# Kernel tuning notes

Hardware: AMD Instinct MI355X
Metric: run time of the kernel (lower is better)

Reference implementation:

```python
import jax, jax.numpy as jnp
import numpy as np
from jax import lax

B, C, K = 16, 320, 8  # batch, channels, template kernel size
EPS = 1e-12  # F.normalize eps


def _pool_to(x, k):
    # adaptive avg pool to (k, k); H, W are exact multiples of k here
    b, c, h, w = x.shape
    return x.reshape(b, c, k, h // k, k, w // k).mean(axis=(3, 5))


def _l2norm(x):
    # L2 normalize over channel dim (dim=1), matching F.normalize(p=2, dim=1)
    n = jnp.sqrt(jnp.sum(x * x, axis=1, keepdims=True))
    return x / jnp.maximum(n, EPS)


def _fusion(feats, w1, b1, w2, b2):
    # global avg pool -> 2-layer MLP score per template -> softmax -> weighted sum
    scores = jnp.concatenate(
        [jax.nn.relu(f.mean(axis=(2, 3)) @ w1 + b1) @ w2 + b2 for f in feats], axis=1
    )  # (B, 3)
    a = jax.nn.softmax(scores, axis=1)
    return sum(a[:, i, None, None, None] * feats[i] for i in range(3))


def _corr(template_kernel, search):
    # depthwise correlation + channel sum == per-sample VALID conv with a
    # single (1, C, K, K) kernel; vmap over batch
    tn = _l2norm(template_kernel)  # (B, C, K, K)
    sn = _l2norm(search)           # (B, C, H, W)

    def one(sb, tb):
        return lax.conv_general_dilated(
            sb[None], tb[None], (1, 1), 'VALID',
            dimension_numbers=('NCHW', 'OIHW', 'NCHW'))[0]  # (1, Ho, Wo)

    return jax.vmap(one)(sn, tn)  # (B, 1, Ho, Wo)


_SPECS = [
    ('t0_p3', (B, C, 32, 32)), ('t0_p4', (B, C, 16, 16)), ('t0_p5', (B, C, 8, 8)),
    ('t1_p3', (B, C, 32, 32)), ('t1_p4', (B, C, 16, 16)), ('t1_p5', (B, C, 8, 8)),
    ('t2_p3', (B, C, 32, 32)), ('t2_p4', (B, C, 16, 16)), ('t2_p5', (B, C, 8, 8)),
    ('s_p3', (B, C, 64, 64)), ('s_p4', (B, C, 32, 32)), ('s_p5', (B, C, 16, 16)),
]
_PARAMS = [
    ('fp3_w1', (C, C // 4)), ('fp3_b1', (C // 4,)), ('fp3_w2', (C // 4, 1)), ('fp3_b2', (1,)),
    ('fp4_w1', (C, C // 4)), ('fp4_b1', (C // 4,)), ('fp4_w2', (C // 4, 1)), ('fp4_b2', (1,)),
    ('fp5_w1', (C, C // 4)), ('fp5_b1', (C // 4,)), ('fp5_w2', (C // 4, 1)), ('fp5_b2', (1,)),
]


def setup_inputs() -> dict:
    key = jax.random.key(0)
    d = {}
    for i, (name, shape) in enumerate(_SPECS):
        d[name] = jax.random.normal(jax.random.fold_in(key, i), shape, jnp.float32)
    for j, (name, shape) in enumerate(_PARAMS):
        k = jax.random.fold_in(key, 100 + j)
        if name.endswith('b1') or name.endswith('b2'):
            d[name] = jnp.zeros(shape, jnp.float32)
        else:
            d[name] = jax.random.normal(k, shape, jnp.float32) * 0.05
    return d


def reference(t0_p3, t0_p4, t0_p5, t1_p3, t1_p4, t1_p5, t2_p3, t2_p4, t2_p5,
              s_p3, s_p4, s_p5,
              fp3_w1, fp3_b1, fp3_w2, fp3_b2,
              fp4_w1, fp4_b1, fp4_w2, fp4_b2,
              fp5_w1, fp5_b1, fp5_w2, fp5_b2):
    tp3 = _fusion([t0_p3, t1_p3, t2_p3], fp3_w1, fp3_b1, fp3_w2, fp3_b2)
    tp4 = _fusion([t0_p4, t1_p4, t2_p4], fp4_w1, fp4_b1, fp4_w2, fp4_b2)
    tp5 = _fusion([t0_p5, t1_p5, t2_p5], fp5_w1, fp5_b1, fp5_w2, fp5_b2)
    corr_p3 = _corr(_pool_to(tp3, K), s_p3)  # (B, 1, 57, 57)
    corr_p4 = _corr(_pool_to(tp4, K), s_p4)  # (B, 1, 25, 25)
    corr_p5 = _corr(_pool_to(tp5, K), s_p5)  # (B, 1, 9, 9)
    return (corr_p3, corr_p4, corr_p5)
```

## Files before the change

### kernel.cpp

```cpp
#include <hip/hip_runtime.h>
#include <math.h>

#define BATCH 16
#define CH 320

typedef __attribute__((ext_vector_type(8))) short bf16x8;
typedef __attribute__((ext_vector_type(4))) float f32x4;

union AFrag { bf16x8 f; unsigned q[4]; };

static constexpr size_t PLSZ     = (size_t)BATCH * CH * 64;
static constexpr size_t WS_POOL3 = 0;
static constexpr size_t WS_POOL4 = 3 * PLSZ;
static constexpr size_t WS_TF    = 6 * PLSZ;
static constexpr size_t WS_MEANS = 9 * PLSZ;
static constexpr size_t WS_AW    = WS_MEANS + 9 * BATCH * CH;
static constexpr size_t WS_PART  = WS_AW + 144;
static constexpr size_t WS_ABF   = WS_PART + 3 * BATCH * 80 * 64;
static constexpr size_t UB3 = 0;
static constexpr size_t UB4 = (size_t)BATCH * 4096 * 64;
static constexpr size_t UB5 = UB4 + (size_t)BATCH * 1024 * 64;

__device__ __forceinline__ float bf2f(unsigned short u) {
    union { unsigned int i; float f; } x; x.i = ((unsigned int)u) << 16; return x.f;
}
__device__ __forceinline__ unsigned short f2bf(float f) {
    union { float f; unsigned int i; } x; x.f = f;
    return (unsigned short)((x.i + 0x7FFFu + ((x.i >> 16) & 1u)) >> 16);
}
__device__ __forceinline__ unsigned cvtpk(float lo, float hi) {
    unsigned r;
    asm("v_cvt_pk_bf16_f32 %0, %1, %2" : "=v"(r) : "v"(lo), "v"(hi));
    return r;
}

template <int HW, int KK>
__device__ __forceinline__ void pool_body(int idx, const float* __restrict__ a0,
                                          const float* __restrict__ a1, const float* __restrict__ a2,
                                          float* __restrict__ dst, float* __restrict__ means, int lane) {
    constexpr int NPL = BATCH * CH * 64;
    int tmpl = idx / NPL;
    int r = idx % NPL;
    const float* src = (tmpl == 0) ? a0 : ((tmpl == 1) ? a1 : a2);
    int bc = r >> 6;
    int pos = r & 63;
    int oh = pos >> 3, ow = pos & 7;
    const float* base = src + (size_t)bc * HW * HW;
    float s = 0.0f;
    if constexpr (KK == 4) {
#pragma unroll
        for (int i = 0; i < 4; ++i) {
            float4 v = *(const float4*)(base + (oh * 4 + i) * HW + ow * 4);
            s += v.x + v.y + v.z + v.w;
        }
    } else {
#pragma unroll
        for (int i = 0; i < 2; ++i) {
            float2 v = *(const float2*)(base + (oh * 2 + i) * HW + ow * 2);
            s += v.x + v.y;
        }
    }
    s *= (1.0f / (KK * KK));
    dst[idx] = s;
    float m = s;
#pragma unroll
    for (int o = 32; o; o >>= 1) m += __shfl_xor(m, o);
    if (lane == 0) means[tmpl * (BATCH * CH) + bc] = m * (1.0f / 64.0f);
}

__global__ __launch_bounds__(256) void prep_kernel(
    const float* __restrict__ t0p3, const float* __restrict__ t1p3, const float* __restrict__ t2p3,
    const float* __restrict__ t0p4, const float* __restrict__ t1p4, const float* __restrict__ t2p4,
    const float* __restrict__ t0p5, const float* __restrict__ t1p5, const float* __restrict__ t2p5,
    float* __restrict__ pool3, float* __restrict__ pool4, float* __restrict__ means) {
    int bid = blockIdx.x, t = threadIdx.x, lane = t & 63;
    if (bid < 3840) {
        pool_body<32, 4>(bid * 256 + t, t0p3, t1p3, t2p3, pool3, means, lane);
    } else if (bid < 7680) {
        pool_body<16, 2>((bid - 3840) * 256 + t, t0p4, t1p4, t2p4, pool4, means + 3 * BATCH * CH, lane);
    } else {
        int w = ((bid - 7680) * 256 + t) >> 6;
        constexpr int NR = BATCH * CH;
        int tmpl = w / NR, rem = w % NR;
        const float* src = (tmpl == 0) ? t0p5 : ((tmpl == 1) ? t1p5 : t2p5);
        float v = src[(size_t)rem * 64 + lane];
#pragma unroll
        for (int o = 32; o; o >>= 1) v += __shfl_xor(v, o);
        if (lane == 0) means[6 * BATCH * CH + w] = v * (1.0f / 64.0f);
    }
}

__global__ __launch_bounds__(256) void weights_kernel(const float* __restrict__ means,
        const float* w13, const float* b13, const float* w23, const float* b23,
        const float* w14, const float* b14, const float* w24, const float* b24,
        const float* w15, const float* b15, const float* w25, const float* b25,
        float* __restrict__ a_out) {
    __shared__ float m[3 * CH];
    __shared__ float hv[240];
    __shared__ float sc[3];
    int lvl = blockIdx.x / BATCH;
    int b = blockIdx.x % BATCH;
    int t = threadIdx.x;
    const float* w1 = (lvl == 0) ? w13 : ((lvl == 1) ? w14 : w15);
    const float* b1 = (lvl == 0) ? b13 : ((lvl == 1) ? b14 : b15);
    const float* w2 = (lvl == 0) ? w23 : ((lvl == 1) ? w24 : w25);
    const float* b2 = (lvl == 0) ? b23 : ((lvl == 1) ? b24 : b25);
    const float* mb = means + lvl * (3 * BATCH * CH);
    for (int j = t; j < 3 * CH; j += 256) {
        int i = j / CH, c = j % CH;
        m[j] = mb[i * (BATCH * CH) + b * CH + c];
    }
    __syncthreads();
    if (t < 240) {
        int i = t / 80, jj = t % 80;
        float acc = b1[jj];
#pragma unroll 4
        for (int c = 0; c < CH; ++c) acc = fmaf(m[i * CH + c], w1[c * 80 + jj], acc);
        hv[t] = fmaxf(acc, 0.0f) * w2[jj];
    }
    __syncthreads();
    if (t < 3) {
        float s = b2[0];
#pragma unroll 8
        for (int jj = 0; jj < 80; ++jj) s += hv[t * 80 + jj];
        sc[t] = s;
    }
    __syncthreads();
    if (t == 0) {
        float mx = fmaxf(sc[0], fmaxf(sc[1], sc[2]));
        float e0 = expf(sc[0] - mx), e1 = expf(sc[1] - mx), e2 = expf(sc[2] - mx);
        float inv = 1.0f / (e0 + e1 + e2);
        float* ao = a_out + lvl * 48 + b * 3;
        ao[0] = e0 * inv; ao[1] = e1 * inv; ao[2] = e2 * inv;
    }
}

__global__ __launch_bounds__(256) void fuse_kernel(
        const float* __restrict__ p30, const float* __restrict__ p31, const float* __restrict__ p32,
        const float* __restrict__ p40, const float* __restrict__ p41, const float* __restrict__ p42,
        const float* __restrict__ p50, const float* __restrict__ p51, const float* __restrict__ p52,
        const float* __restrict__ aw, float* __restrict__ tf, float* __restrict__ partial) {
    __shared__ float red[256];
    int lvl = blockIdx.x / 1280;
    int r = blockIdx.x % 1280;
    int t = threadIdx.x;
    const float* p0 = (lvl == 0) ? p30 : ((lvl == 1) ? p40 : p50);
    const float* p1 = (lvl == 0) ? p31 : ((lvl == 1) ? p41 : p51);
    const float* p2 = (lvl == 0) ? p32 : ((lvl == 1) ? p42 : p52);
    int idx = r * 256 + t;
    int b = r / 80;
    int j = r % 80;
    const float* ab = aw + lvl * 48 + b * 3;
    float a0 = ab[0], a1 = ab[1], a2 = ab[2];
    float v = a0 * p0[idx] + a1 * p1[idx] + a2 * p2[idx];
    tf[(size_t)lvl * PLSZ + idx] = v;
    red[t] = v * v;
    __syncthreads();
    if (t < 64) {
        float s = red[t] + red[t + 64] + red[t + 128] + red[t + 192];
        partial[((size_t)(lvl * BATCH + b) * 80 + j) * 64 + t] = s;
    }
}

__global__ __launch_bounds__(256) void atrans_kernel(const float* __restrict__ tf,
        const float* __restrict__ part, short* __restrict__ abf) {
    __shared__ float lds[64 * 68];
    __shared__ float red2[4 * 64];
    __shared__ float sv[64];
    int lvl = blockIdx.x >> 4;
    int b = blockIdx.x & 15;
    int t = threadIdx.x;
    {
        const float* p = part + ((size_t)(lvl * BATCH + b) * 80) * 64 + (t & 63);
        int jg = t >> 6;
        float s = 0.0f;
        for (int j = jg * 20; j < jg * 20 + 20; ++j) s += p[j * 64];
        red2[jg * 64 + (t & 63)] = s;
    }
    __syncthreads();
    if (t < 64) {
        float s = red2[t] + red2[64 + t] + red2[128 + t] + red2[192 + t];
        sv[t] = 1.0f / fmaxf(sqrtf(s), 1e-12f);
    }
    __syncthreads();
    const float* tb = tf + (size_t)lvl * PLSZ + (size_t)b * (CH * 64);
    short* ab = abf + ((size_t)(lvl * BATCH + b) * 64) * 320;
    for (int c0 = 0; c0 < 320; c0 += 64) {
        __syncthreads();
#pragma unroll
        for (int i = 0; i < 4; ++i) {
            int c = (t >> 4) + 16 * i;
            int p4 = (t & 15) * 4;
            *(float4*)(lds + c * 68 + p4) = *(const float4*)(tb + (size_t)(c0 + c) * 64 + p4);
        }
        __syncthreads();
        int p = t >> 2;
        int cs = (t & 3) * 16;
        float s_p = sv[p];
        bf16x8 o0, o1;
#pragma unroll
        for (int u = 0; u < 8; ++u) o0[u] = (short)f2bf(lds[(cs + u) * 68 + p] * s_p);
#pragma unroll
        for (int u = 0; u < 8; ++u) o1[u] = (short)f2bf(lds[(cs + 8 + u) * 68 + p] * s_p);
        *(bf16x8*)(ab + (size_t)p * 320 + c0 + cs) = o0;
        *(bf16x8*)(ab + (size_t)p * 320 + c0 + cs + 8) = o1;
    }
}

template <int H>
__device__ __forceinline__ void gemm_body(const float* __restrict__ S, const short* __restrict__ T,
                                          short* __restrict__ V, int bid) {
    constexpr int N = H * H;
    constexpr int XB = N / 64;
    int b = bid / XB;
    int x0b = (bid % XB) * 64;
    int t = threadIdx.x;
    int w = t >> 6, l = t & 63, g = l >> 4, ln = l & 15;
    int xw = x0b + 16 * w;

    const float* Sb = S + (size_t)b * CH * N + xw + ln;
    const short* Tb = T + (size_t)b * 64 * 320;

    f32x4 acc[4];
#pragma unroll
    for (int i = 0; i < 4; ++i) acc[i] = (f32x4){0.f, 0.f, 0.f, 0.f};
    float ssq = 0.0f;

#pragma unroll
    for (int s = 0; s < 10; ++s) {
        int c0 = 32 * s + 8 * g;
        float av[8];
#pragma unroll
        for (int j = 0; j < 8; ++j) av[j] = Sb[(size_t)(c0 + j) * N];
        bf16x8 tb0 = *(const bf16x8*)(Tb + (size_t)(0 * 16 + ln) * 320 + c0);
        bf16x8 tb1 = *(const bf16x8*)(Tb + (size_t)(1 * 16 + ln) * 320 + c0);
        bf16x8 tb2 = *(const bf16x8*)(Tb + (size_t)(2 * 16 + ln) * 320 + c0);
        bf16x8 tb3 = *(const bf16x8*)(Tb + (size_t)(3 * 16 + ln) * 320 + c0);
#pragma unroll
        for (int j = 0; j < 8; ++j) ssq = fmaf(av[j], av[j], ssq);
        AFrag fa;
        fa.q[0] = cvtpk(av[0], av[1]);
        fa.q[1] = cvtpk(av[2], av[3]);
        fa.q[2] = cvtpk(av[4], av[5]);
        fa.q[3] = cvtpk(av[6], av[7]);
        acc[0] = __builtin_amdgcn_mfma_f32_16x16x32_bf16(fa.f, tb0, acc[0], 0, 0, 0);
        acc[1] = __builtin_amdgcn_mfma_f32_16x16x32_bf16(fa.f, tb1, acc[1], 0, 0, 0);
        acc[2] = __builtin_amdgcn_mfma_f32_16x16x32_bf16(fa.f, tb2, acc[2], 0, 0, 0);
        acc[3] = __builtin_amdgcn_mfma_f32_16x16x32_bf16(fa.f, tb3, acc[3], 0, 0, 0);
    }

    ssq += __shfl_xor(ssq, 16);
    ssq += __shfl_xor(ssq, 32);
    float inv = 1.0f / fmaxf(sqrtf(ssq), 1e-12f);
    float iv[4];
#pragma unroll
    for (int r = 0; r < 4; ++r) iv[r] = __shfl(inv, 4 * g + r);

#pragma unroll
    for (int pt = 0; pt < 4; ++pt)
#pragma unroll
        for (int r = 0; r < 4; ++r)
            V[((size_t)b * N + xw + 4 * g + r) * 64 + pt * 16 + ln] =
                (short)f2bf(acc[pt][r] * iv[r]);
}

__global__ __launch_bounds__(256, 4) void gemm_kernel(const float* __restrict__ sp3,
        const float* __restrict__ sp4, const float* __restrict__ sp5,
        const short* __restrict__ abf, short* __restrict__ u) {
    int bid = blockIdx.x;
    if (bid < 1024)      gemm_body<64>(sp3, abf,          u + UB3, bid);
    else if (bid < 1280) gemm_body<32>(sp4, abf + 327680, u + UB4, bid - 1024);
    else                 gemm_body<16>(sp5, abf + 655360, u + UB5, bid - 1280);
}

__global__ __launch_bounds__(256) void combine_kernel(const short* __restrict__ U,
                                                      float* __restrict__ out) {
    int tid = blockIdx.x * 256 + threadIdx.x;
    if (tid < 51984) {
        int b = tid / 3249, r = tid % 3249;
        int oh = r / 57, ow = r % 57;
        const short* u = U + UB3 + ((size_t)b * 4096 + oh * 64 + ow) * 64;
        float s = 0.0f;
#pragma unroll
        for (int kh = 0; kh < 8; ++kh)
#pragma unroll
            for (int kw = 0; kw < 8; ++kw)
                s += bf2f((unsigned short)u[(kh * 64 + kw) * 64 + kh * 8 + kw]);
        out[tid] = s;
    } else if (tid < 61984) {
        int x = tid - 51984;
        int b = x / 625, r = x % 625;
        int oh = r / 25, ow = r % 25;
        const short* u = U + UB4 + ((size_t)b * 1024 + oh * 32 + ow) * 64;
        float s = 0.0f;
#pragma unroll
        for (int kh = 0; kh < 8; ++kh)
#pragma unroll
            for (int kw = 0; kw < 8; ++kw)
                s += bf2f((unsigned short)u[(kh * 32 + kw) * 64 + kh * 8 + kw]);
        out[tid] = s;
    } else if (tid < 63280) {
        int x = tid - 61984;
        int b = x / 81, r = x % 81;
        int oh = r / 9, ow = r % 9;
        const short* u = U + UB5 + ((size_t)b * 256 + oh * 16 + ow) * 64;
        float s = 0.0f;
#pragma unroll
        for (int kh = 0; kh < 8; ++kh)
#pragma unroll
            for (int kw = 0; kw < 8; ++kw)
                s += bf2f((unsigned short)u[(kh * 16 + kw) * 64 + kh * 8 + kw]);
        out[tid] = s;
    }
}

extern "C" void kernel_launch(void* const* d_in, const int* in_sizes, int n_in,
                              void* d_out, int out_size, void* d_ws, size_t ws_size,
                              hipStream_t stream) {
    const float* t0p3 = (const float*)d_in[0];
    const float* t0p4 = (const float*)d_in[1];
    const float* t0p5 = (const float*)d_in[2];
    const float* t1p3 = (const float*)d_in[3];
    const float* t1p4 = (const float*)d_in[4];
    const float* t1p5 = (const float*)d_in[5];
    const float* t2p3 = (const float*)d_in[6];
    const float* t2p4 = (const float*)d_in[7];
    const float* t2p5 = (const float*)d_in[8];
    const float* sp3  = (const float*)d_in[9];
    const float* sp4  = (const float*)d_in[10];
    const float* sp5  = (const float*)d_in[11];
    const float* f3w1 = (const float*)d_in[12];
    const float* f3b1 = (const float*)d_in[13];
    const float* f3w2 = (const float*)d_in[14];
    const float* f3b2 = (const float*)d_in[15];
    const float* f4w1 = (const float*)d_in[16];
    const float* f4b1 = (const float*)d_in[17];
    const float* f4w2 = (const float*)d_in[18];
    const float* f4b2 = (const float*)d_in[19];
    const float* f5w1 = (const float*)d_in[20];
    const float* f5b1 = (const float*)d_in[21];
    const float* f5w2 = (const float*)d_in[22];
    const float* f5b2 = (const float*)d_in[23];

    float* ws = (float*)d_ws;
    short* abf = (short*)(ws + WS_ABF);
    short* ubuf = (short*)ws;

    prep_kernel<<<11520, 256, 0, stream>>>(t0p3, t1p3, t2p3, t0p4, t1p4, t2p4,
                                           t0p5, t1p5, t2p5,
                                           ws + WS_POOL3, ws + WS_POOL4, ws + WS_MEANS);
    weights_kernel<<<48, 256, 0, stream>>>(ws + WS_MEANS,
                                           f3w1, f3b1, f3w2, f3b2,
                                           f4w1, f4b1, f4w2, f4b2,
                                           f5w1, f5b1, f5w2, f5b2, ws + WS_AW);
    fuse_kernel<<<3840, 256, 0, stream>>>(ws + WS_POOL3, ws + WS_POOL3 + PLSZ, ws + WS_POOL3 + 2 * PLSZ,
                                          ws + WS_POOL4, ws + WS_POOL4 + PLSZ, ws + WS_POOL4 + 2 * PLSZ,
                                          t0p5, t1p5, t2p5,
                                          ws + WS_AW, ws + WS_TF, ws + WS_PART);
    atrans_kernel<<<48, 256, 0, stream>>>(ws + WS_TF, ws + WS_PART, abf);
    gemm_kernel<<<1344, 256, 0, stream>>>(sp3, sp4, sp5, abf, ubuf);
    combine_kernel<<<248, 256, 0, stream>>>(ubuf, (float*)d_out);
}
```

Before: 99.82 us.

## Stage search tiles through double-buffered LDS with transpose reads in GEMM

The GEMM kernel now handles 128 spatial positions per block instead of 64. Search features are read with coalesced float4 loads, converted to bf16 and written into a double-buffered LDS tile. MFMA A-fragments are then read back with ds_read_b64_tr_b16 transpose loads. The next channel slice's global loads are prefetched while the current slice is multiplied, and the per-position L2 norm is reduced through shared memory. This aims to replace strided scalar global loads with coalesced vector loads and to overlap memory with compute, at the cost of LDS use, extra barriers, half as many blocks, and inline asm that waits on lgkmcnt(0) before each MFMA pair.

Result: slower. 118.7 us (+18.9%).

```diff
diff --git a/kernel.cpp b/kernel.cpp
--- a/kernel.cpp
+++ b/kernel.cpp
@@ -7,7 +7,7 @@
 typedef __attribute__((ext_vector_type(8))) short bf16x8;
 typedef __attribute__((ext_vector_type(4))) float f32x4;
 
-union AFrag { bf16x8 f; unsigned q[4]; };
+union FragU { bf16x8 f; unsigned long long u[2]; };
 
 static constexpr size_t PLSZ     = (size_t)BATCH * CH * 64;
 static constexpr size_t WS_POOL3 = 0;
@@ -209,68 +209,129 @@
 
 template <int H>
 __device__ __forceinline__ void gemm_body(const float* __restrict__ S, const short* __restrict__ T,
-                                          short* __restrict__ V, int bid) {
+                                          short* __restrict__ V, int bid,
+                                          unsigned short* St, float* red, float* invs) {
     constexpr int N = H * H;
-    constexpr int XB = N / 64;
+    constexpr int XB = N / 128;
     int b = bid / XB;
-    int x0b = (bid % XB) * 64;
+    int x0b = (bid % XB) * 128;
     int t = threadIdx.x;
     int w = t >> 6, l = t & 63, g = l >> 4, ln = l & 15;
-    int xw = x0b + 16 * w;
-
-    const float* Sb = S + (size_t)b * CH * N + xw + ln;
-    const short* Tb = T + (size_t)b * 64 * 320;
-
-    f32x4 acc[4];
-#pragma unroll
-    for (int i = 0; i < 4; ++i) acc[i] = (f32x4){0.f, 0.f, 0.f, 0.f};
-    float ssq = 0.0f;
+    int fidx = l & 31;
+    int rsub = l >> 5;
+    int h = fidx >> 4;
+
+    const float* Sp = S + (size_t)b * CH * N + x0b + fidx * 4;
+    const short* Tp = T + ((size_t)b * 64 + (w >> 1) * 32 + ln) * 320 + 8 * g;
+
+    f32x4 acc[4][2];
+#pragma unroll
+    for (int i = 0; i < 4; ++i)
+#pragma unroll
+        for (int j = 0; j < 2; ++j) acc[i][j] = (f32x4){0.f, 0.f, 0.f, 0.f};
+    float ssq[4] = {0.f, 0.f, 0.f, 0.f};
+
+    unsigned trbase = (unsigned)(size_t)St * 2u;
+    trbase = (unsigned)(size_t)St;
+    trbase = (unsigned)(size_t)(St) + (unsigned)((w & 1) * 4096 + g * 256 + ln * 8);
+
+    int ebase[4];
+#pragma unroll
+    for (int i = 0; i < 4; ++i) {
+        int cl = w * 8 + 2 * i + rsub;
+        ebase[i] = h * 2048 + (((fidx & 15) >> 2) * 8 + (cl >> 2)) * 64 + (cl & 3) * 16 + (fidx & 3) * 4;
+    }
+
+#define LOADS(PV, S_) { \
+    _Pragma("unroll") \
+    for (int i = 0; i < 4; ++i) \
+        PV[i] = *(const float4*)(Sp + (size_t)(32 * (S_) + w * 8 + 2 * i + rsub) * N); }
+
+#define STAGE(PV, BUF) { \
+    _Pragma("unroll") \
+    for (int i = 0; i < 4; ++i) { \
+        float4 v = PV[i]; \
+        ssq[0] = fmaf(v.x, v.x, ssq[0]); ssq[1] = fmaf(v.y, v.y, ssq[1]); \
+        ssq[2] = fmaf(v.z, v.z, ssq[2]); ssq[3] = fmaf(v.w, v.w, ssq[3]); \
+        *(uint2*)(St + (BUF) * 4096 + ebase[i]) = (uint2){cvtpk(v.x, v.y), cvtpk(v.z, v.w)}; \
+    } }
+
+#define TRRD2(FR, OFF) \
+    asm volatile("ds_read_b64_tr_b16 %0, %2 offset:%c3\n\tds_read_b64_tr_b16 %1, %2 offset:%c4" \
+                 : "=v"((FR).u[0]), "=v"((FR).u[1]) : "v"(trbase), "i"(OFF), "i"((OFF) + 128));
+
+    float4 cv[4];
+    LOADS(cv, 0)
+    bf16x8 cta = *(const bf16x8*)(Tp);
+    bf16x8 ctb = *(const bf16x8*)(Tp + 5120);
+    STAGE(cv, 0)
+    __syncthreads();
 
 #pragma unroll
     for (int s = 0; s < 10; ++s) {
-        int c0 = 32 * s + 8 * g;
-        float av[8];
-#pragma unroll
-        for (int j = 0; j < 8; ++j) av[j] = Sb[(size_t)(c0 + j) * N];
-        bf16x8 tb0 = *(const bf16x8*)(Tb + (size_t)(0 * 16 + ln) * 320 + c0);
-        bf16x8 tb1 = *(const bf16x8*)(Tb + (size_t)(1 * 16 + ln) * 320 + c0);
-        bf16x8 tb2 = *(const bf16x8*)(Tb + (size_t)(2 * 16 + ln) * 320 + c0);
-        bf16x8 tb3 = *(const bf16x8*)(Tb + (size_t)(3 * 16 + ln) * 320 + c0);
-#pragma unroll
-        for (int j = 0; j < 8; ++j) ssq = fmaf(av[j], av[j], ssq);
-        AFrag fa;
-        fa.q[0] = cvtpk(av[0], av[1]);
-        fa.q[1] = cvtpk(av[2], av[3]);
-        fa.q[2] = cvtpk(av[4], av[5]);
-        fa.q[3] = cvtpk(av[6], av[7]);
-        acc[0] = __builtin_amdgcn_mfma_f32_16x16x32_bf16(fa.f, tb0, acc[0], 0, 0, 0);
-        acc[1] = __builtin_amdgcn_mfma_f32_16x16x32_bf16(fa.f, tb1, acc[1], 0, 0, 0);
-        acc[2] = __builtin_amdgcn_mfma_f32_16x16x32_bf16(fa.f, tb2, acc[2], 0, 0, 0);
-        acc[3] = __builtin_amdgcn_mfma_f32_16x16x32_bf16(fa.f, tb3, acc[3], 0, 0, 0);
-    }
-
-    ssq += __shfl_xor(ssq, 16);
-    ssq += __shfl_xor(ssq, 32);
-    float inv = 1.0f / fmaxf(sqrtf(ssq), 1e-12f);
-    float iv[4];
-#pragma unroll
-    for (int r = 0; r < 4; ++r) iv[r] = __shfl(inv, 4 * g + r);
-
-#pragma unroll
-    for (int pt = 0; pt < 4; ++pt)
-#pragma unroll
-        for (int r = 0; r < 4; ++r)
-            V[((size_t)b * N + xw + 4 * g + r) * 64 + pt * 16 + ln] =
-                (short)f2bf(acc[pt][r] * iv[r]);
+        const int cur = s & 1;
+        float4 nv[4];
+        bf16x8 nta, ntb;
+        if (s < 9) {
+            LOADS(nv, s + 1)
+            nta = *(const bf16x8*)(Tp + 32 * (s + 1));
+            ntb = *(const bf16x8*)(Tp + 5120 + 32 * (s + 1));
+        }
+#pragma unroll
+        for (int mt = 0; mt < 4; ++mt) {
+            FragU fr;
+            TRRD2(fr, 0 + mt * 1024)
+            ;
+            asm volatile("s_waitcnt lgkmcnt(0)" ::: "memory");
+            __builtin_amdgcn_sched_barrier(0);
+            acc[mt][0] = __builtin_amdgcn_mfma_f32_16x16x32_bf16(fr.f, cta, acc[mt][0], 0, 0, 0);
+            acc[mt][1] = __builtin_amdgcn_mfma_f32_16x16x32_bf16(fr.f, ctb, acc[mt][1], 0, 0, 0);
+        }
+        if (s < 9) {
+            STAGE(nv, cur ^ 1)
+            cta = nta; ctb = ntb;
+        }
+        __syncthreads();
+        trbase ^= 8192u;
+    }
+#undef TRRD2
+#undef STAGE
+#undef LOADS
+
+    int grp = w * 2 + rsub;
+    *(f32x4*)(red + grp * 128 + fidx * 4) = (f32x4){ssq[0], ssq[1], ssq[2], ssq[3]};
+    __syncthreads();
+    if (t < 128) {
+        float s = 0.0f;
+#pragma unroll
+        for (int i = 0; i < 8; ++i) s += red[i * 128 + t];
+        invs[t] = 1.0f / fmaxf(sqrtf(s), 1e-12f);
+    }
+    __syncthreads();
+
+#pragma unroll
+    for (int mt = 0; mt < 4; ++mt) {
+#pragma unroll
+        for (int r = 0; r < 4; ++r) {
+            int xl = (w & 1) * 64 + mt * 16 + 4 * g + r;
+            float iv = invs[xl];
+            short* vp = V + ((size_t)b * N + x0b + xl) * 64 + (w >> 1) * 32 + ln;
+            vp[0]  = (short)f2bf(acc[mt][0][r] * iv);
+            vp[16] = (short)f2bf(acc[mt][1][r] * iv);
+        }
+    }
 }
 
 __global__ __launch_bounds__(256, 4) void gemm_kernel(const float* __restrict__ sp3,
         const float* __restrict__ sp4, const float* __restrict__ sp5,
         const short* __restrict__ abf, short* __restrict__ u) {
+    __shared__ unsigned short St[2 * 4096];
+    __shared__ float red[8 * 128];
+    __shared__ float invs[128];
     int bid = blockIdx.x;
-    if (bid < 1024)      gemm_body<64>(sp3, abf,          u + UB3, bid);
-    else if (bid < 1280) gemm_body<32>(sp4, abf + 327680, u + UB4, bid - 1024);
-    else                 gemm_body<16>(sp5, abf + 655360, u + UB5, bid - 1280);
+    if (bid < 512)      gemm_body<64>(sp3, abf,          u + UB3, bid,       St, red, invs);
+    else if (bid < 640) gemm_body<32>(sp4, abf + 327680, u + UB4, bid - 512, St, red, invs);
+    else                gemm_body<16>(sp5, abf + 655360, u + UB5, bid - 640, St, red, invs);
 }
 
 __global__ __launch_bounds__(256) void combine_kernel(const short* __restrict__ U,
@@ -358,6 +419,6 @@
                                           t0p5, t1p5, t2p5,
                                           ws + WS_AW, ws + WS_TF, ws + WS_PART);
     atrans_kernel<<<48, 256, 0, stream>>>(ws + WS_TF, ws + WS_PART, abf);
-    gemm_kernel<<<1344, 256, 0, stream>>>(sp3, sp4, sp5, abf, ubuf);
+    gemm_kernel<<<672, 256, 0, stream>>>(sp3, sp4, sp5, abf, ubuf);
     combine_kernel<<<248, 256, 0, stream>>>(ubuf, (float*)d_out);
 }
```
